# Kernel optimization log

Measured on AMD Instinct MI355X. Metric: run time of the kernel, lower is better.

The kernel has to match this reference:

```python
import jax, jax.numpy as jnp
import numpy as np

NPOINT = 2048
RADIUS = 0.4
NSAMPLE = 32
EPS = 1e-5  # BatchNorm eps


def setup_inputs() -> dict:
    key = jax.random.key(0)
    ks = jax.random.split(key, 16)
    B, N, Cf = 8, 8192, 6
    xyz = jax.random.uniform(ks[0], (B, 3, N), jnp.float32)        # coords in unit cube
    points = jax.random.normal(ks[1], (B, Cf, N), jnp.float32)     # per-point features
    inp = {"xyz": xyz, "points": points}
    dims = [9, 64, 64, 128]  # in_channel=3+Cf, mlp=[64,64,128]
    for i in range(3):
        cin, cout = dims[i], dims[i + 1]
        bound = 1.0 / np.sqrt(cin)
        inp[f"w{i+1}"] = jax.random.uniform(ks[2 + 4 * i], (cout, cin), jnp.float32, -bound, bound)
        inp[f"b{i+1}"] = jax.random.uniform(ks[3 + 4 * i], (cout,), jnp.float32, -bound, bound)
        inp[f"g{i+1}"] = jnp.ones((cout,), jnp.float32)   # BN gamma
        inp[f"be{i+1}"] = jnp.zeros((cout,), jnp.float32)  # BN beta
    return inp


def _fps(pts):
    """Furthest point sampling. pts: (N,3) -> (NPOINT,) int32 indices (first index is 0)."""
    N = pts.shape[0]

    def step(carry, _):
        dist, last = carry
        d = jnp.sum((pts - pts[last]) ** 2, axis=-1)
        dist = jnp.minimum(dist, d)
        nxt = jnp.argmax(dist).astype(jnp.int32)
        return (dist, nxt), last

    init = (jnp.full((N,), 1e10, pts.dtype), jnp.int32(0))
    _, idx = jax.lax.scan(step, init, None, length=NPOINT)
    return idx


def _ball_query(new_xyz_t, xyz_t):
    """Indices of up to NSAMPLE points within RADIUS of each centroid; empty slots
    replicate the first in-ball index (pointnet2_ops semantics).
    new_xyz_t: (B,S,3), xyz_t: (B,N,3) -> (B,S,NSAMPLE) int32."""
    N = xyz_t.shape[1]
    sq = jnp.sum((new_xyz_t[:, :, None, :] - xyz_t[:, None, :, :]) ** 2, axis=-1)  # (B,S,N)
    mask = sq <= RADIUS ** 2
    # key = own index if in ball else N -> stable argsort yields in-ball indices in order
    keys = jnp.where(mask, jnp.arange(N, dtype=jnp.int32), jnp.int32(N))
    order = jnp.argsort(keys, axis=-1)[..., :NSAMPLE].astype(jnp.int32)            # (B,S,K)
    cnt = jnp.sum(mask, axis=-1)                                                   # (B,S)
    valid = jnp.arange(NSAMPLE, dtype=jnp.int32)[None, None, :] < cnt[..., None]
    return jnp.where(valid, order, order[..., :1])


def _forward(xyz, points, params):
    xyz_t = jnp.transpose(xyz, (0, 2, 1))          # (B,N,3)
    pts_t = jnp.transpose(points, (0, 2, 1))       # (B,N,C)

    fps_idx = jax.vmap(_fps)(xyz_t)                # (B,S)
    gather = jax.vmap(lambda p, i: p[i])
    new_xyz_t = gather(xyz_t, fps_idx)             # (B,S,3)

    idx = _ball_query(new_xyz_t, xyz_t)            # (B,S,K)
    grouped_xyz = gather(xyz_t, idx) - new_xyz_t[:, :, None, :]   # (B,S,K,3) centered
    grouped_pts = gather(pts_t, idx)                              # (B,S,K,C)
    feat = jnp.concatenate([grouped_xyz, grouped_pts], axis=-1)   # (B,S,K,3+C)
    x = jnp.transpose(feat, (0, 3, 1, 2))                         # (B,Cin,S,K)

    for (w, b, g, be) in params:
        x = jnp.einsum('oc,bcsk->bosk', w, x) + b[None, :, None, None]  # 1x1 conv
        mu = jnp.mean(x, axis=(0, 2, 3), keepdims=True)                  # BN (batch stats)
        var = jnp.mean((x - mu) ** 2, axis=(0, 2, 3), keepdims=True)
        x = (x - mu) * jax.lax.rsqrt(var + EPS) * g[None, :, None, None] + be[None, :, None, None]
        x = jax.nn.relu(x)

    new_points = jnp.max(x, axis=-1)               # (B,D,S) max over nsample
    new_xyz = jnp.transpose(new_xyz_t, (0, 2, 1))  # (B,3,S)
    return new_xyz, new_points


def reference(xyz, points, w1, b1, g1, be1, w2, b2, g2, be2, w3, b3, g3, be3):
    params = [(w1, b1, g1, be1), (w2, b2, g2, be2), (w3, b3, g3, be3)]
    return _forward(xyz, points, params)
```

## Files before the change

### kernel.cpp

```cpp
#include <hip/hip_runtime.h>
#include <cstdint>

#define N_PTS   8192
#define S_PTS   2048
#define K_SMP   32
#define BATCH   8
#define P_TOT   (BATCH*S_PTS*K_SMP)
#define R2      0.16f
#define CNT_INV (1.0f/524288.0f)

__device__ __forceinline__ float sqd(float ax, float ay, float az,
                                     float bx, float by, float bz) {
    float dx = __fsub_rn(ax, bx), dy = __fsub_rn(ay, by), dz = __fsub_rn(az, bz);
    return __fadd_rn(__fadd_rn(__fmul_rn(dx, dx), __fmul_rn(dy, dy)), __fmul_rn(dz, dz));
}

#define ROR_STEP(N)                                                                         \
    {                                                                                       \
        float ov = __int_as_float(__builtin_amdgcn_mov_dpp(__float_as_int(bv),              \
                                                           0x120|(N), 0xF, 0xF, true));     \
        int   oi = __builtin_amdgcn_mov_dpp(bi, 0x120|(N), 0xF, 0xF, true);                 \
        if (ov > bv || (ov == bv && oi < bi)) { bv = ov; bi = oi; }                         \
    }
#define XOR_STEP(N)                                                                         \
    {                                                                                       \
        float ov = __shfl_xor(bv, N);                                                       \
        int   oi = __shfl_xor(bi, N);                                                       \
        if (ov > bv || (ov == bv && oi < bi)) { bv = ov; bi = oi; }                         \
    }

__global__ __launch_bounds__(512) void fps_kernel(const float* __restrict__ xyz,
                                                  float* __restrict__ newxyz) {
    __shared__ float4 pts[N_PTS];
    __shared__ unsigned long long s_part[2][8];
    __shared__ int s_sel[S_PTS];

    const int b = blockIdx.x, t = threadIdx.x;
    const int w = t >> 6, lane = t & 63;
    const float* xb = xyz + (size_t)b * 3 * N_PTS;
    const int base = t * 16;

    float px[16], py[16], pz[16], dist[16];
#pragma unroll
    for (int q = 0; q < 4; q++) {
        float4 vx = *(const float4*)(xb + base + 4 * q);
        float4 vy = *(const float4*)(xb + N_PTS + base + 4 * q);
        float4 vz = *(const float4*)(xb + 2 * N_PTS + base + 4 * q);
        px[4*q] = vx.x; px[4*q+1] = vx.y; px[4*q+2] = vx.z; px[4*q+3] = vx.w;
        py[4*q] = vy.x; py[4*q+1] = vy.y; py[4*q+2] = vy.z; py[4*q+3] = vy.w;
        pz[4*q] = vz.x; pz[4*q+1] = vz.y; pz[4*q+2] = vz.z; pz[4*q+3] = vz.w;
    }
#pragma unroll
    for (int j = 0; j < 16; j++) {
        pts[base+j] = make_float4(px[j], py[j], pz[j], 0.f);
        dist[j] = 1e10f;
    }
    if (t == 0) s_sel[0] = 0;
    __syncthreads();

    int last = 0;
    for (int i = 1; i < S_PTS; i++) {
        float4 L = pts[last];
        float lx = L.x, ly = L.y, lz = L.z;
        float bv = -1.0f;
#pragma unroll
        for (int j = 0; j < 16; j++) {
            float dx = px[j] - lx, dy = py[j] - ly, dz = pz[j] - lz;
            float d  = __fmaf_rn(dz, dz, __fmaf_rn(dy, dy, __fmul_rn(dx, dx)));
            float nd = fminf(dist[j], d);
            dist[j] = nd;
            bv = fmaxf(bv, nd);
        }
        int bi = base;
#pragma unroll
        for (int j = 15; j >= 0; j--) if (dist[j] == bv) bi = base + j;

        ROR_STEP(1) ROR_STEP(2) ROR_STEP(4) ROR_STEP(8)
        XOR_STEP(16) XOR_STEP(32)
        if (lane == 0)
            s_part[i & 1][w] = ((unsigned long long)__float_as_uint(bv) << 32)
                             | (unsigned long long)(0xFFFFFFFFu - (unsigned)bi);
        __syncthreads();
        const unsigned long long* sp = s_part[i & 1];
        unsigned long long best = sp[0];
#pragma unroll
        for (int r = 1; r < 8; r++) { unsigned long long k = sp[r]; if (k > best) best = k; }
        last = (int)(0xFFFFFFFFu - (unsigned)(best & 0xFFFFFFFFull)) & (N_PTS - 1);
        if (t == 0) s_sel[i] = last;
    }
    __syncthreads();
    for (int s = t; s < S_PTS; s += 512) {
        float4 P = pts[s_sel[s]];
        newxyz[((size_t)b*3 + 0) * S_PTS + s] = P.x;
        newxyz[((size_t)b*3 + 1) * S_PTS + s] = P.y;
        newxyz[((size_t)b*3 + 2) * S_PTS + s] = P.z;
    }
}

__global__ __launch_bounds__(256) void ball_kernel(const float* __restrict__ xyz,
                                                   const float* __restrict__ newxyz,
                                                   int* __restrict__ ballidx) {
    int g    = blockIdx.x * 4 + (threadIdx.x >> 6);
    int lane = threadIdx.x & 63;
    int b = g >> 11, s = g & 2047;
    const float* xb = xyz + (size_t)b * 3 * N_PTS;
    float cx = newxyz[((size_t)b*3 + 0) * S_PTS + s];
    float cy = newxyz[((size_t)b*3 + 1) * S_PTS + s];
    float cz = newxyz[((size_t)b*3 + 2) * S_PTS + s];
    int* outp = ballidx + (size_t)g * K_SMP;

    int cnt = 0, first = 0;  bool have_first = false;
    for (int n0 = 0; n0 < N_PTS; n0 += 64) {
        int n = n0 + lane;
        float d = sqd(cx, cy, cz, xb[n], xb[N_PTS + n], xb[2*N_PTS + n]);
        bool in = (d <= R2);
        unsigned long long m = __ballot(in);
        if (in) {
            int pos = cnt + __popcll(m & ((1ull << lane) - 1ull));
            if (pos < K_SMP) outp[pos] = n;
        }
        if (!have_first && m != 0ull) { first = n0 + (int)__builtin_ctzll(m); have_first = true; }
        cnt += __popcll(m);
        if (cnt >= K_SMP) break;
    }
    if (cnt < K_SMP && lane < K_SMP && lane >= cnt) outp[lane] = first;
}

__global__ __launch_bounds__(256) void d_conv1(const float* __restrict__ xyz,
                                               const float* __restrict__ points,
                                               const float* __restrict__ newxyz,
                                               const int* __restrict__ ballidx,
                                               const float* __restrict__ w1,
                                               const float* __restrict__ b1,
                                               float* __restrict__ xbuf) {
    __shared__ float sw[64 * 9];
    __shared__ float sb[64];
    int t = threadIdx.x;
    for (int i = t; i < 576; i += 256) sw[i] = w1[i];
    if (t < 64) sb[t] = b1[t];
    __syncthreads();

    int p = blockIdx.x * 256 + t;
    int g = p >> 5, b = g >> 11, s = g & 2047;
    int idx = ballidx[p] & (N_PTS - 1);
    const float* xb = xyz    + (size_t)b * 3 * N_PTS;
    const float* pb = points + (size_t)b * 6 * N_PTS;
    float f[9];
    f[0] = xb[idx]           - newxyz[((size_t)b*3 + 0) * S_PTS + s];
    f[1] = xb[N_PTS + idx]   - newxyz[((size_t)b*3 + 1) * S_PTS + s];
    f[2] = xb[2*N_PTS + idx] - newxyz[((size_t)b*3 + 2) * S_PTS + s];
#pragma unroll
    for (int c = 0; c < 6; c++) f[3 + c] = pb[c * N_PTS + idx];

    float* row = xbuf + (size_t)p * 64;
    for (int co = 0; co < 64; co++) {
        float a = sb[co];
#pragma unroll
        for (int c = 0; c < 9; c++) a += sw[co * 9 + c] * f[c];
        row[co] = a;
    }
}

template <int C>
__global__ __launch_bounds__(256) void d_stats(const float* __restrict__ x,
                                               float* __restrict__ gstat) {
    __shared__ float ss[C], sq[C];
    int t = threadIdx.x;
    for (int i = t; i < C; i += 256) { ss[i] = 0.f; sq[i] = 0.f; }
    __syncthreads();
    int c = t & (C - 1), r0 = t / C;
    const int RPI = 256 / C;
    float s = 0.f, q = 0.f;
    size_t base = (size_t)blockIdx.x * 256;
    for (int r = r0; r < 256; r += RPI) {
        float v = x[(base + r) * C + c];
        s += v; q += v * v;
    }
    atomicAdd(&ss[c], s); atomicAdd(&sq[c], q);
    __syncthreads();
    for (int i = t; i < C; i += 256) { atomicAdd(&gstat[i], ss[i]); atomicAdd(&gstat[C + i], sq[i]); }
}

__global__ __launch_bounds__(256) void c2_kernel(float* __restrict__ xbuf,
                                                 const float* __restrict__ AB1,
                                                 const float* __restrict__ w2,
                                                 const float* __restrict__ b2) {
    __shared__ __align__(16) float wt[64 * 64];
    __shared__ float sA[64], sB[64], sb[64];
    int t = threadIdx.x;
    for (int i = t; i < 4096; i += 256) { int co = i & 63, c = i >> 6; wt[c*64+co] = w2[co*64+c]; }
    if (t < 64) { sA[t] = AB1[t]; sB[t] = AB1[64 + t]; sb[t] = b2[t]; }
    __syncthreads();

    size_t p0 = (size_t)blockIdx.x * 512 + t, p1 = p0 + 256;
    float* r0 = xbuf + p0 * 64;
    float* r1 = xbuf + p1 * 64;

    float acc0[64], acc1[64];
#pragma unroll
    for (int co = 0; co < 64; co++) { float bv = sb[co]; acc0[co] = bv; acc1[co] = bv; }

#pragma unroll
    for (int c0 = 0; c0 < 64; c0 += 8) {
        float ya[8], yb[8];
#pragma unroll
        for (int q = 0; q < 8; q += 4) {
            float4 va = *(const float4*)(r0 + c0 + q);
            float4 vb = *(const float4*)(r1 + c0 + q);
            ya[q] = va.x; ya[q+1] = va.y; ya[q+2] = va.z; ya[q+3] = va.w;
            yb[q] = vb.x; yb[q+1] = vb.y; yb[q+2] = vb.z; yb[q+3] = vb.w;
        }
#pragma unroll
        for (int q = 0; q < 8; q++) {
            ya[q] = fmaxf(0.f, ya[q] * sA[c0+q] + sB[c0+q]);
            yb[q] = fmaxf(0.f, yb[q] * sA[c0+q] + sB[c0+q]);
        }
#pragma unroll
        for (int c = 0; c < 8; c++) {
            float fa = ya[c], fb = yb[c];
#pragma unroll
            for (int co = 0; co < 64; co += 4) {
                float4 w = *(const float4*)&wt[(c0+c)*64 + co];
                acc0[co]   += w.x * fa; acc0[co+1] += w.y * fa;
                acc0[co+2] += w.z * fa; acc0[co+3] += w.w * fa;
                acc1[co]   += w.x * fb; acc1[co+1] += w.y * fb;
                acc1[co+2] += w.z * fb; acc1[co+3] += w.w * fb;
            }
        }
    }
#pragma unroll
    for (int co = 0; co < 64; co += 4) {
        *(float4*)(r0 + co) = make_float4(acc0[co], acc0[co+1], acc0[co+2], acc0[co+3]);
        *(float4*)(r1 + co) = make_float4(acc1[co], acc1[co+1], acc1[co+2], acc1[co+3]);
    }
}

#define C3_COMPUTE(ACC)                                                                    \
    int quarter = t & 3, q = t >> 2, cb = quarter * 32;                                    \
    size_t pB = (size_t)blockIdx.x * 256 + q;                                              \
    const float* r0 = xbuf + (pB +   0) * 64;                                              \
    const float* r1 = xbuf + (pB +  64) * 64;                                              \
    const float* r2 = xbuf + (pB + 128) * 64;                                              \
    const float* r3 = xbuf + (pB + 192) * 64;                                              \
    float ACC[4][32];                                                                      \
    _Pragma("unroll")                                                                      \
    for (int co = 0; co < 32; co++) {                                                      \
        float bv = sb3[cb + co];                                                           \
        ACC[0][co] = bv; ACC[1][co] = bv; ACC[2][co] = bv; ACC[3][co] = bv;                \
    }                                                                                      \
    _Pragma("unroll")                                                                      \
    for (int c0 = 0; c0 < 64; c0 += 8) {                                                   \
        float y[4][8];                                                                     \
        _Pragma("unroll")                                                                  \
        for (int qq = 0; qq < 8; qq += 4) {                                                \
            float4 v0 = *(const float4*)(r0 + c0 + qq);                                    \
            float4 v1 = *(const float4*)(r1 + c0 + qq);                                    \
            float4 v2 = *(const float4*)(r2 + c0 + qq);                                    \
            float4 v3 = *(const float4*)(r3 + c0 + qq);                                    \
            y[0][qq] = v0.x; y[0][qq+1] = v0.y; y[0][qq+2] = v0.z; y[0][qq+3] = v0.w;      \
            y[1][qq] = v1.x; y[1][qq+1] = v1.y; y[1][qq+2] = v1.z; y[1][qq+3] = v1.w;      \
            y[2][qq] = v2.x; y[2][qq+1] = v2.y; y[2][qq+2] = v2.z; y[2][qq+3] = v2.w;      \
            y[3][qq] = v3.x; y[3][qq+1] = v3.y; y[3][qq+2] = v3.z; y[3][qq+3] = v3.w;      \
        }                                                                                  \
        _Pragma("unroll")                                                                  \
        for (int qq = 0; qq < 8; qq++) {                                                   \
            float A = sA[c0+qq], Bv = sB[c0+qq];                                           \
            y[0][qq] = fmaxf(0.f, y[0][qq] * A + Bv);                                      \
            y[1][qq] = fmaxf(0.f, y[1][qq] * A + Bv);                                      \
            y[2][qq] = fmaxf(0.f, y[2][qq] * A + Bv);                                      \
            y[3][qq] = fmaxf(0.f, y[3][qq] * A + Bv);                                      \
        }                                                                                  \
        _Pragma("unroll")                                                                  \
        for (int c = 0; c < 8; c++) {                                                      \
            float f0 = y[0][c], f1 = y[1][c], f2 = y[2][c], f3 = y[3][c];                  \
            _Pragma("unroll")                                                              \
            for (int co = 0; co < 32; co += 4) {                                           \
                float4 w = *(const float4*)&wt[(c0+c)*128 + cb + co];                      \
                ACC[0][co]   += w.x * f0; ACC[0][co+1] += w.y * f0;                        \
                ACC[0][co+2] += w.z * f0; ACC[0][co+3] += w.w * f0;                        \
                ACC[1][co]   += w.x * f1; ACC[1][co+1] += w.y * f1;                        \
                ACC[1][co+2] += w.z * f1; ACC[1][co+3] += w.w * f1;                        \
                ACC[2][co]   += w.x * f2; ACC[2][co+1] += w.y * f2;                        \
                ACC[2][co+2] += w.z * f2; ACC[2][co+3] += w.w * f2;                        \
                ACC[3][co]   += w.x * f3; ACC[3][co+1] += w.y * f3;                        \
                ACC[3][co+2] += w.z * f3; ACC[3][co+3] += w.w * f3;                        \
            }                                                                              \
        }                                                                                  \
    }

__global__ __launch_bounds__(256) void c3_stats(const float* __restrict__ xbuf,
                                                const float* __restrict__ AB2,
                                                const float* __restrict__ w3,
                                                const float* __restrict__ b3,
                                                float* __restrict__ gstat) {
    __shared__ __align__(16) float wt[64 * 128];
    __shared__ float sA[64], sB[64], sb3[128], ss[128], sq[128];
    int t = threadIdx.x;
    for (int i = t; i < 8192; i += 256) { int ch = i & 127, c = i >> 7; wt[c*128+ch] = w3[ch*64+c]; }
    if (t < 64) { sA[t] = AB2[t]; sB[t] = AB2[64 + t]; }
    if (t < 128) { sb3[t] = b3[t]; ss[t] = 0.f; sq[t] = 0.f; }
    __syncthreads();

    C3_COMPUTE(acc)

#pragma unroll
    for (int co = 0; co < 32; co++) {
        float s  = acc[0][co] + acc[1][co] + acc[2][co] + acc[3][co];
        float qq = acc[0][co]*acc[0][co] + acc[1][co]*acc[1][co]
                 + acc[2][co]*acc[2][co] + acc[3][co]*acc[3][co];
        atomicAdd(&ss[cb + co], s);
        atomicAdd(&sq[cb + co], qq);
    }
    __syncthreads();
    if (t < 128) { atomicAdd(&gstat[t], ss[t]); atomicAdd(&gstat[128 + t], sq[t]); }
}

__global__ __launch_bounds__(256) void c3_max(const float* __restrict__ xbuf,
                                              const float* __restrict__ AB2,
                                              const float* __restrict__ w3,
                                              const float* __restrict__ b3,
                                              const float* __restrict__ AB3,
                                              float* __restrict__ out_np) {
    __shared__ __align__(16) float wt[64 * 128];
    __shared__ float sA[64], sB[64], sb3[128], sA3[128], sB3[128];
    __shared__ unsigned int smax[8][128];
    int t = threadIdx.x;
    for (int i = t; i < 8192; i += 256) { int ch = i & 127, c = i >> 7; wt[c*128+ch] = w3[ch*64+c]; }
    if (t < 64) { sA[t] = AB2[t]; sB[t] = AB2[64 + t]; }
    if (t < 128) { sb3[t] = b3[t]; sA3[t] = AB3[t]; sB3[t] = AB3[128 + t]; }
    for (int i = t; i < 1024; i += 256) smax[i >> 7][i & 127] = 0u;
    __syncthreads();

    C3_COMPUTE(acc)

    int g0 = (q >> 5);
#pragma unroll
    for (int co = 0; co < 32; co++) {
        int ch = cb + co;
        float A = sA3[ch], Bv = sB3[ch];
        float v0 = fmaxf(0.f, acc[0][co] * A + Bv);
        float v1 = fmaxf(0.f, acc[1][co] * A + Bv);
        float v2 = fmaxf(0.f, acc[2][co] * A + Bv);
        float v3 = fmaxf(0.f, acc[3][co] * A + Bv);
        atomicMax(&smax[g0    ][ch], __float_as_uint(v0));
        atomicMax(&smax[g0 + 2][ch], __float_as_uint(v1));
        atomicMax(&smax[g0 + 4][ch], __float_as_uint(v2));
        atomicMax(&smax[g0 + 6][ch], __float_as_uint(v3));
    }
    __syncthreads();
    for (int i = t; i < 1024; i += 256) {
        int g = i >> 7, ch = i & 127;
        int G = blockIdx.x * 8 + g;
        int b = G >> 11, s = G & 2047;
        out_np[((size_t)b * 128 + ch) * 2048 + s] = __uint_as_float(smax[g][ch]);
    }
}

template <int C>
__global__ void finalize_kernel(const float* __restrict__ gstat,
                                const float* __restrict__ gamma,
                                const float* __restrict__ beta,
                                float* __restrict__ AB) {
    int t = threadIdx.x;
    if (t < C) {
        float mu  = gstat[t]     * CNT_INV;
        float ex2 = gstat[C + t] * CNT_INV;
        float var = ex2 - mu * mu;
        float A = gamma[t] * rsqrtf(var + 1e-5f);
        AB[t] = A; AB[C + t] = beta[t] - mu * A;
    }
}

extern "C" void kernel_launch(void* const* d_in, const int* in_sizes, int n_in,
                              void* d_out, int out_size, void* d_ws, size_t ws_size,
                              hipStream_t stream) {
    (void)in_sizes; (void)n_in; (void)out_size; (void)ws_size;
    const float* xyz    = (const float*)d_in[0];
    const float* points = (const float*)d_in[1];
    const float* w1 = (const float*)d_in[2],  *b1 = (const float*)d_in[3];
    const float* g1 = (const float*)d_in[4],  *be1 = (const float*)d_in[5];
    const float* w2 = (const float*)d_in[6],  *b2 = (const float*)d_in[7];
    const float* g2 = (const float*)d_in[8],  *be2 = (const float*)d_in[9];
    const float* w3 = (const float*)d_in[10], *b3 = (const float*)d_in[11];
    const float* g3 = (const float*)d_in[12], *be3 = (const float*)d_in[13];

    float* out    = (float*)d_out;
    float* out_np = out + (size_t)BATCH * 3 * S_PTS;

    char*  ws      = (char*)d_ws;
    int*   ballidx = (int*)ws;
    float* gbase   = (float*)(ws + (2ull << 20));
    float* gstat1  = gbase;
    float* gstat2  = gbase + 256;
    float* gstat3  = gbase + 512;
    float* AB1     = gbase + 768;
    float* AB2     = gbase + 896;
    float* AB3     = gbase + 1024;
    float* xbuf    = (float*)(ws + (4ull << 20));

    hipMemsetAsync(gstat1, 0, 768 * sizeof(float), stream);

    fps_kernel  <<<BATCH, 512, 0, stream>>>(xyz, out);
    ball_kernel <<<(BATCH * S_PTS) / 4, 256, 0, stream>>>(xyz, out, ballidx);
    d_conv1     <<<P_TOT / 256, 256, 0, stream>>>(xyz, points, out, ballidx, w1, b1, xbuf);
    d_stats<64> <<<P_TOT / 256, 256, 0, stream>>>(xbuf, gstat1);
    finalize_kernel<64><<<1, 64, 0, stream>>>(gstat1, g1, be1, AB1);
    c2_kernel   <<<P_TOT / 512, 256, 0, stream>>>(xbuf, AB1, w2, b2);
    d_stats<64> <<<P_TOT / 256, 256, 0, stream>>>(xbuf, gstat2);
    finalize_kernel<64><<<1, 64, 0, stream>>>(gstat2, g2, be2, AB2);
    c3_stats    <<<P_TOT / 256, 256, 0, stream>>>(xbuf, AB2, w3, b3, gstat3);
    finalize_kernel<128><<<1, 128, 0, stream>>>(gstat3, g3, be3, AB3);
    c3_max      <<<P_TOT / 256, 256, 0, stream>>>(xbuf, AB2, w3, b3, AB3, out_np);
}
```

Before: 3.343 ms.

## Transpose activations to channel-major and derive layer-3 BN stats from Gram matrix

Switches the intermediate activation buffer from point-major to channel-major layout, so per-channel loads and stores coalesce across threads and the stats reduction becomes contiguous float4 streaming. Replaces the full layer-3 conv pass used only for batch statistics with a 64x64 Gram matrix and channel sums of the layer-2 outputs. The layer-3 mean and variance are then computed algebraically from the weights and bias in a small finalize kernel. This avoids one 64->128 matmul pass, but adds many global float atomics on the Gram matrix and accepts possible precision loss from computing variance as E[x^2] with large sums.

```diff
diff --git a/kernel.cpp b/kernel.cpp
--- a/kernel.cpp
+++ b/kernel.cpp
@@ -132,7 +132,7 @@
                                                const int* __restrict__ ballidx,
                                                const float* __restrict__ w1,
                                                const float* __restrict__ b1,
-                                               float* __restrict__ xbuf) {
+                                               float* __restrict__ xT) {
     __shared__ float sw[64 * 9];
     __shared__ float sb[64];
     int t = threadIdx.x;
@@ -152,36 +152,36 @@
 #pragma unroll
     for (int c = 0; c < 6; c++) f[3 + c] = pb[c * N_PTS + idx];
 
-    float* row = xbuf + (size_t)p * 64;
     for (int co = 0; co < 64; co++) {
         float a = sb[co];
 #pragma unroll
         for (int c = 0; c < 9; c++) a += sw[co * 9 + c] * f[c];
-        row[co] = a;
-    }
-}
-
-template <int C>
-__global__ __launch_bounds__(256) void d_stats(const float* __restrict__ x,
-                                               float* __restrict__ gstat) {
-    __shared__ float ss[C], sq[C];
-    int t = threadIdx.x;
-    for (int i = t; i < C; i += 256) { ss[i] = 0.f; sq[i] = 0.f; }
-    __syncthreads();
-    int c = t & (C - 1), r0 = t / C;
-    const int RPI = 256 / C;
+        xT[(size_t)co * P_TOT + p] = a;
+    }
+}
+
+__global__ __launch_bounds__(256) void d_statsT(const float* __restrict__ xT,
+                                                float* __restrict__ gstat) {
+    __shared__ float ls[2];
+    int t = threadIdx.x;
+    if (t < 2) ls[t] = 0.f;
+    __syncthreads();
+    int c = blockIdx.x >> 3, sl = blockIdx.x & 7;
+    const float* base = xT + (size_t)c * P_TOT + sl * 65536;
     float s = 0.f, q = 0.f;
-    size_t base = (size_t)blockIdx.x * 256;
-    for (int r = r0; r < 256; r += RPI) {
-        float v = x[(base + r) * C + c];
-        s += v; q += v * v;
-    }
-    atomicAdd(&ss[c], s); atomicAdd(&sq[c], q);
-    __syncthreads();
-    for (int i = t; i < C; i += 256) { atomicAdd(&gstat[i], ss[i]); atomicAdd(&gstat[C + i], sq[i]); }
-}
-
-__global__ __launch_bounds__(256) void c2_kernel(float* __restrict__ xbuf,
+    for (int i = t * 4; i < 65536; i += 1024) {
+        float4 v = *(const float4*)(base + i);
+        s += v.x + v.y + v.z + v.w;
+        q += v.x*v.x + v.y*v.y + v.z*v.z + v.w*v.w;
+    }
+#pragma unroll
+    for (int off = 1; off <= 32; off <<= 1) { s += __shfl_xor(s, off); q += __shfl_xor(q, off); }
+    if ((t & 63) == 0) { atomicAdd(&ls[0], s); atomicAdd(&ls[1], q); }
+    __syncthreads();
+    if (t == 0) { atomicAdd(&gstat[c], ls[0]); atomicAdd(&gstat[64 + c], ls[1]); }
+}
+
+__global__ __launch_bounds__(256) void c2_kernel(float* __restrict__ xT,
                                                  const float* __restrict__ AB1,
                                                  const float* __restrict__ w2,
                                                  const float* __restrict__ b2) {
@@ -193,8 +193,6 @@
     __syncthreads();
 
     size_t p0 = (size_t)blockIdx.x * 512 + t, p1 = p0 + 256;
-    float* r0 = xbuf + p0 * 64;
-    float* r1 = xbuf + p1 * 64;
 
     float acc0[64], acc1[64];
 #pragma unroll
@@ -204,11 +202,9 @@
     for (int c0 = 0; c0 < 64; c0 += 8) {
         float ya[8], yb[8];
 #pragma unroll
-        for (int q = 0; q < 8; q += 4) {
-            float4 va = *(const float4*)(r0 + c0 + q);
-            float4 vb = *(const float4*)(r1 + c0 + q);
-            ya[q] = va.x; ya[q+1] = va.y; ya[q+2] = va.z; ya[q+3] = va.w;
-            yb[q] = vb.x; yb[q+1] = vb.y; yb[q+2] = vb.z; yb[q+3] = vb.w;
+        for (int q = 0; q < 8; q++) {
+            ya[q] = xT[(size_t)(c0+q) * P_TOT + p0];
+            yb[q] = xT[(size_t)(c0+q) * P_TOT + p1];
         }
 #pragma unroll
         for (int q = 0; q < 8; q++) {
@@ -229,93 +225,85 @@
         }
     }
 #pragma unroll
-    for (int co = 0; co < 64; co += 4) {
-        *(float4*)(r0 + co) = make_float4(acc0[co], acc0[co+1], acc0[co+2], acc0[co+3]);
-        *(float4*)(r1 + co) = make_float4(acc1[co], acc1[co+1], acc1[co+2], acc1[co+3]);
-    }
-}
-
-#define C3_COMPUTE(ACC)                                                                    \
-    int quarter = t & 3, q = t >> 2, cb = quarter * 32;                                    \
-    size_t pB = (size_t)blockIdx.x * 256 + q;                                              \
-    const float* r0 = xbuf + (pB +   0) * 64;                                              \
-    const float* r1 = xbuf + (pB +  64) * 64;                                              \
-    const float* r2 = xbuf + (pB + 128) * 64;                                              \
-    const float* r3 = xbuf + (pB + 192) * 64;                                              \
-    float ACC[4][32];                                                                      \
-    _Pragma("unroll")                                                                      \
-    for (int co = 0; co < 32; co++) {                                                      \
-        float bv = sb3[cb + co];                                                           \
-        ACC[0][co] = bv; ACC[1][co] = bv; ACC[2][co] = bv; ACC[3][co] = bv;                \
-    }                                                                                      \
-    _Pragma("unroll")                                                                      \
-    for (int c0 = 0; c0 < 64; c0 += 8) {                                                   \
-        float y[4][8];                                                                     \
-        _Pragma("unroll")                                                                  \
-        for (int qq = 0; qq < 8; qq += 4) {                                                \
-            float4 v0 = *(const float4*)(r0 + c0 + qq);                                    \
-            float4 v1 = *(const float4*)(r1 + c0 + qq);                                    \
-            float4 v2 = *(const float4*)(r2 + c0 + qq);                                    \
-            float4 v3 = *(const float4*)(r3 + c0 + qq);                                    \
-            y[0][qq] = v0.x; y[0][qq+1] = v0.y; y[0][qq+2] = v0.z; y[0][qq+3] = v0.w;      \
-            y[1][qq] = v1.x; y[1][qq+1] = v1.y; y[1][qq+2] = v1.z; y[1][qq+3] = v1.w;      \
-            y[2][qq] = v2.x; y[2][qq+1] = v2.y; y[2][qq+2] = v2.z; y[2][qq+3] = v2.w;      \
-            y[3][qq] = v3.x; y[3][qq+1] = v3.y; y[3][qq+2] = v3.z; y[3][qq+3] = v3.w;      \
-        }                                                                                  \
-        _Pragma("unroll")                                                                  \
-        for (int qq = 0; qq < 8; qq++) {                                                   \
-            float A = sA[c0+qq], Bv = sB[c0+qq];                                           \
-            y[0][qq] = fmaxf(0.f, y[0][qq] * A + Bv);                                      \
-            y[1][qq] = fmaxf(0.f, y[1][qq] * A + Bv);                                      \
-            y[2][qq] = fmaxf(0.f, y[2][qq] * A + Bv);                                      \
-            y[3][qq] = fmaxf(0.f, y[3][qq] * A + Bv);                                      \
-        }                                                                                  \
-        _Pragma("unroll")                                                                  \
-        for (int c = 0; c < 8; c++) {                                                      \
-            float f0 = y[0][c], f1 = y[1][c], f2 = y[2][c], f3 = y[3][c];                  \
-            _Pragma("unroll")                                                              \
-            for (int co = 0; co < 32; co += 4) {                                           \
-                float4 w = *(const float4*)&wt[(c0+c)*128 + cb + co];                      \
-                ACC[0][co]   += w.x * f0; ACC[0][co+1] += w.y * f0;                        \
-                ACC[0][co+2] += w.z * f0; ACC[0][co+3] += w.w * f0;                        \
-                ACC[1][co]   += w.x * f1; ACC[1][co+1] += w.y * f1;                        \
-                ACC[1][co+2] += w.z * f1; ACC[1][co+3] += w.w * f1;                        \
-                ACC[2][co]   += w.x * f2; ACC[2][co+1] += w.y * f2;                        \
-                ACC[2][co+2] += w.z * f2; ACC[2][co+3] += w.w * f2;                        \
-                ACC[3][co]   += w.x * f3; ACC[3][co+1] += w.y * f3;                        \
-                ACC[3][co+2] += w.z * f3; ACC[3][co+3] += w.w * f3;                        \
-            }                                                                              \
-        }                                                                                  \
-    }
-
-__global__ __launch_bounds__(256) void c3_stats(const float* __restrict__ xbuf,
-                                                const float* __restrict__ AB2,
-                                                const float* __restrict__ w3,
-                                                const float* __restrict__ b3,
-                                                float* __restrict__ gstat) {
-    __shared__ __align__(16) float wt[64 * 128];
-    __shared__ float sA[64], sB[64], sb3[128], ss[128], sq[128];
-    int t = threadIdx.x;
-    for (int i = t; i < 8192; i += 256) { int ch = i & 127, c = i >> 7; wt[c*128+ch] = w3[ch*64+c]; }
+    for (int co = 0; co < 64; co++) {
+        xT[(size_t)co * P_TOT + p0] = acc0[co];
+        xT[(size_t)co * P_TOT + p1] = acc1[co];
+    }
+}
+
+__global__ __launch_bounds__(256) void c3m_kernel(const float* __restrict__ xT,
+                                                  const float* __restrict__ AB2,
+                                                  float* __restrict__ M3,
+                                                  float* __restrict__ S3) {
+    __shared__ __align__(16) float zb[256][68];
+    __shared__ float sA[64], sB[64];
+    int t = threadIdx.x;
     if (t < 64) { sA[t] = AB2[t]; sB[t] = AB2[64 + t]; }
-    if (t < 128) { sb3[t] = b3[t]; ss[t] = 0.f; sq[t] = 0.f; }
-    __syncthreads();
-
-    C3_COMPUTE(acc)
-
-#pragma unroll
-    for (int co = 0; co < 32; co++) {
-        float s  = acc[0][co] + acc[1][co] + acc[2][co] + acc[3][co];
-        float qq = acc[0][co]*acc[0][co] + acc[1][co]*acc[1][co]
-                 + acc[2][co]*acc[2][co] + acc[3][co]*acc[3][co];
-        atomicAdd(&ss[cb + co], s);
-        atomicAdd(&sq[cb + co], qq);
-    }
-    __syncthreads();
-    if (t < 128) { atomicAdd(&gstat[t], ss[t]); atomicAdd(&gstat[128 + t], sq[t]); }
-}
-
-__global__ __launch_bounds__(256) void c3_max(const float* __restrict__ xbuf,
+    __syncthreads();
+
+    int i0 = (t >> 4) * 4, j0 = (t & 15) * 4;
+    float m00=0,m01=0,m02=0,m03=0,m10=0,m11=0,m12=0,m13=0;
+    float m20=0,m21=0,m22=0,m23=0,m30=0,m31=0,m32=0,m33=0;
+    float ssum = 0.f;
+
+    for (int chunk = 0; chunk < 4; chunk++) {
+        size_t p = (size_t)blockIdx.x * 1024 + chunk * 256 + t;
+        for (int c = 0; c < 64; c++) {
+            float v = xT[(size_t)c * P_TOT + p];
+            zb[t][c] = fmaxf(0.f, v * sA[c] + sB[c]);
+        }
+        __syncthreads();
+        for (int r = 0; r < 256; r++) {
+            float4 zi = *(const float4*)&zb[r][i0];
+            float4 zj = *(const float4*)&zb[r][j0];
+            m00 += zi.x*zj.x; m01 += zi.x*zj.y; m02 += zi.x*zj.z; m03 += zi.x*zj.w;
+            m10 += zi.y*zj.x; m11 += zi.y*zj.y; m12 += zi.y*zj.z; m13 += zi.y*zj.w;
+            m20 += zi.z*zj.x; m21 += zi.z*zj.y; m22 += zi.z*zj.z; m23 += zi.z*zj.w;
+            m30 += zi.w*zj.x; m31 += zi.w*zj.y; m32 += zi.w*zj.z; m33 += zi.w*zj.w;
+        }
+        if (t >= 192) { int ch = t - 192; for (int r = 0; r < 256; r++) ssum += zb[r][ch]; }
+        __syncthreads();
+    }
+    atomicAdd(&M3[(i0+0)*64 + j0+0], m00); atomicAdd(&M3[(i0+0)*64 + j0+1], m01);
+    atomicAdd(&M3[(i0+0)*64 + j0+2], m02); atomicAdd(&M3[(i0+0)*64 + j0+3], m03);
+    atomicAdd(&M3[(i0+1)*64 + j0+0], m10); atomicAdd(&M3[(i0+1)*64 + j0+1], m11);
+    atomicAdd(&M3[(i0+1)*64 + j0+2], m12); atomicAdd(&M3[(i0+1)*64 + j0+3], m13);
+    atomicAdd(&M3[(i0+2)*64 + j0+0], m20); atomicAdd(&M3[(i0+2)*64 + j0+1], m21);
+    atomicAdd(&M3[(i0+2)*64 + j0+2], m22); atomicAdd(&M3[(i0+2)*64 + j0+3], m23);
+    atomicAdd(&M3[(i0+3)*64 + j0+0], m30); atomicAdd(&M3[(i0+3)*64 + j0+1], m31);
+    atomicAdd(&M3[(i0+3)*64 + j0+2], m32); atomicAdd(&M3[(i0+3)*64 + j0+3], m33);
+    if (t >= 192) atomicAdd(&S3[t - 192], ssum);
+}
+
+__global__ void finalizeM3_kernel(const float* __restrict__ M3,
+                                  const float* __restrict__ S3,
+                                  const float* __restrict__ w3,
+                                  const float* __restrict__ b3,
+                                  float* __restrict__ gstat3) {
+    __shared__ float sM[4096], sS[64];
+    int t = threadIdx.x;
+    for (int i = t; i < 4096; i += 128) sM[i] = M3[i];
+    if (t < 64) sS[t] = S3[t];
+    __syncthreads();
+
+    float wv[64];
+#pragma unroll
+    for (int j = 0; j < 64; j++) wv[j] = w3[t * 64 + j];
+    float b = b3[t];
+    float dot = 0.f, quad = 0.f;
+    for (int i = 0; i < 64; i++) {
+        float di = 0.f;
+        const float* Mr = &sM[i * 64];
+#pragma unroll
+        for (int j = 0; j < 64; j++) di += Mr[j] * wv[j];
+        quad += wv[i] * di;
+        dot  += wv[i] * sS[i];
+    }
+    gstat3[t]       = dot + (float)P_TOT * b;
+    gstat3[128 + t] = quad + 2.f * b * dot + (float)P_TOT * b * b;
+}
+
+__global__ __launch_bounds__(256) void c3_max(const float* __restrict__ xT,
                                               const float* __restrict__ AB2,
                                               const float* __restrict__ w3,
                                               const float* __restrict__ b3,
@@ -331,8 +319,51 @@
     for (int i = t; i < 1024; i += 256) smax[i >> 7][i & 127] = 0u;
     __syncthreads();
 
-    C3_COMPUTE(acc)
-
+    int quarter = t & 3, q = t >> 2, cb = quarter * 32;
+    size_t pB = (size_t)blockIdx.x * 256 + q;
+
+    float acc[4][32];
+#pragma unroll
+    for (int co = 0; co < 32; co++) {
+        float bv = sb3[cb + co];
+        acc[0][co] = bv; acc[1][co] = bv; acc[2][co] = bv; acc[3][co] = bv;
+    }
+#pragma unroll
+    for (int c0 = 0; c0 < 64; c0 += 8) {
+        float y[4][8];
+#pragma unroll
+        for (int qq = 0; qq < 8; qq++) {
+            const float* col = xT + (size_t)(c0+qq) * P_TOT + pB;
+            y[0][qq] = col[0];
+            y[1][qq] = col[64];
+            y[2][qq] = col[128];
+            y[3][qq] = col[192];
+        }
+#pragma unroll
+        for (int qq = 0; qq < 8; qq++) {
+            float A = sA[c0+qq], Bv = sB[c0+qq];
+            y[0][qq] = fmaxf(0.f, y[0][qq] * A + Bv);
+            y[1][qq] = fmaxf(0.f, y[1][qq] * A + Bv);
+            y[2][qq] = fmaxf(0.f, y[2][qq] * A + Bv);
+            y[3][qq] = fmaxf(0.f, y[3][qq] * A + Bv);
+        }
+#pragma unroll
+        for (int c = 0; c < 8; c++) {
+            float f0 = y[0][c], f1 = y[1][c], f2 = y[2][c], f3 = y[3][c];
+#pragma unroll
+            for (int co = 0; co < 32; co += 4) {
+                float4 w = *(const float4*)&wt[(c0+c)*128 + cb + co];
+                acc[0][co]   += w.x * f0; acc[0][co+1] += w.y * f0;
+                acc[0][co+2] += w.z * f0; acc[0][co+3] += w.w * f0;
+                acc[1][co]   += w.x * f1; acc[1][co+1] += w.y * f1;
+                acc[1][co+2] += w.z * f1; acc[1][co+3] += w.w * f1;
+                acc[2][co]   += w.x * f2; acc[2][co+1] += w.y * f2;
+                acc[2][co+2] += w.z * f2; acc[2][co+3] += w.w * f2;
+                acc[3][co]   += w.x * f3; acc[3][co+1] += w.y * f3;
+                acc[3][co+2] += w.z * f3; acc[3][co+3] += w.w * f3;
+            }
+        }
+    }
     int g0 = (q >> 5);
 #pragma unroll
     for (int co = 0; co < 32; co++) {
@@ -396,19 +427,22 @@
     float* AB1     = gbase + 768;
     float* AB2     = gbase + 896;
     float* AB3     = gbase + 1024;
-    float* xbuf    = (float*)(ws + (4ull << 20));
-
-    hipMemsetAsync(gstat1, 0, 768 * sizeof(float), stream);
+    float* M3      = gbase + 1280;
+    float* S3      = gbase + 5376;
+    float* xT      = (float*)(ws + (4ull << 20));
+
+    hipMemsetAsync(gbase, 0, 5440 * sizeof(float), stream);
 
     fps_kernel  <<<BATCH, 512, 0, stream>>>(xyz, out);
     ball_kernel <<<(BATCH * S_PTS) / 4, 256, 0, stream>>>(xyz, out, ballidx);
-    d_conv1     <<<P_TOT / 256, 256, 0, stream>>>(xyz, points, out, ballidx, w1, b1, xbuf);
-    d_stats<64> <<<P_TOT / 256, 256, 0, stream>>>(xbuf, gstat1);
+    d_conv1     <<<P_TOT / 256, 256, 0, stream>>>(xyz, points, out, ballidx, w1, b1, xT);
+    d_statsT    <<<512, 256, 0, stream>>>(xT, gstat1);
     finalize_kernel<64><<<1, 64, 0, stream>>>(gstat1, g1, be1, AB1);
-    c2_kernel   <<<P_TOT / 512, 256, 0, stream>>>(xbuf, AB1, w2, b2);
-    d_stats<64> <<<P_TOT / 256, 256, 0, stream>>>(xbuf, gstat2);
+    c2_kernel   <<<P_TOT / 512, 256, 0, stream>>>(xT, AB1, w2, b2);
+    d_statsT    <<<512, 256, 0, stream>>>(xT, gstat2);
     finalize_kernel<64><<<1, 64, 0, stream>>>(gstat2, g2, be2, AB2);
-    c3_stats    <<<P_TOT / 256, 256, 0, stream>>>(xbuf, AB2, w3, b3, gstat3);
+    c3m_kernel  <<<512, 256, 0, stream>>>(xT, AB2, M3, S3);
+    finalizeM3_kernel<<<1, 128, 0, stream>>>(M3, S3, w3, b3, gstat3);
     finalize_kernel<128><<<1, 128, 0, stream>>>(gstat3, g3, be3, AB3);
-    c3_max      <<<P_TOT / 256, 256, 0, stream>>>(xbuf, AB2, w3, b3, AB3, out_np);
-}
+    c3_max      <<<P_TOT / 256, 256, 0, stream>>>(xT, AB2, w3, b3, AB3, out_np);
+}
```

New measurement: 3.043 ms. 1.1x faster.
